# Kernel optimization log

Hardware: AMD Instinct MI355X
Metric: run time of the kernel (lower is better)

The kernel has to match this reference:

```python
import jax, jax.numpy as jnp
import numpy as np

B, C, H, W = 4, 512, 64, 64
IC = C // 2  # inter_plane
EPS = 1e-5


def _conv1x1(x, w, b=None):
    # x: [b,c,h,w], w: [o,c] -> [b,o,h,w]
    y = jnp.einsum('bchw,oc->bohw', x, w)
    if b is not None:
        y = y + b[None, :, None, None]
    return y


def setup_inputs() -> dict:
    key = jax.random.key(0)
    ks = jax.random.split(key, 20)
    rn = lambda i, sh, s=0.02: jax.random.normal(ks[i], sh, jnp.float32) * s
    return {
        'xA': jax.random.normal(ks[0], (B, C, H, W), jnp.float32),
        'wk': rn(1, (IC, C)), 'bk': rn(2, (IC,)),
        'wv': rn(3, (IC, C)), 'bv': rn(4, (IC,)),
        'wq': rn(5, (IC, C)), 'bq': rn(6, (IC,)),
        'wwg': rn(7, (IC, IC)),
        'bn1_g': jnp.ones((IC,), jnp.float32), 'bn1_b': rn(8, (IC,)),
        'bn1_m': rn(9, (IC,)), 'bn1_v': jax.random.uniform(ks[10], (IC,), jnp.float32, 0.5, 1.5),
        'wout': rn(11, (C, IC)), 'bout': rn(12, (C,)),
        'bn2_g': jnp.ones((C,), jnp.float32), 'bn2_b': rn(13, (C,)),
        'bn2_m': rn(14, (C,)), 'bn2_v': jax.random.uniform(ks[15], (C,), jnp.float32, 0.5, 1.5),
    }


def reference(xA, wk, bk, wv, bv, wq, bq, wwg, bn1_g, bn1_b, bn1_m, bn1_v,
              wout, bout, bn2_g, bn2_b, bn2_m, bn2_v):
    b, c, h, w = xA.shape
    n = h * w
    k = _conv1x1(xA, wk, bk).reshape(b, IC, n)   # [b,ic,n]
    v = _conv1x1(xA, wv, bv).reshape(b, IC, n)   # [b,ic,n] (permuted via einsum below)
    q = _conv1x1(xA, wq, bq).reshape(b, IC, n)   # [b,ic,n]
    # AV = softmax(v^T @ q, axis=2): [b,n,n]
    attn = jax.nn.softmax(jnp.einsum('bcn,bcm->bnm', v, q), axis=2)
    av = jnp.einsum('bcn,bnm->bcm', k, attn)     # [b,ic,n]
    # conv1d 1x1 (no bias) + BatchNorm1d (eval mode)
    avw = jnp.einsum('oc,bcn->bon', wwg, av)
    scale1 = bn1_g / jnp.sqrt(bn1_v + EPS)
    avw = (avw - bn1_m[None, :, None]) * scale1[None, :, None] + bn1_b[None, :, None]
    avw = avw.reshape(b, IC, h, w)
    # out conv + BatchNorm2d (eval) + residual + relu
    o = _conv1x1(avw, wout, bout)
    scale2 = bn2_g / jnp.sqrt(bn2_v + EPS)
    o = (o - bn2_m[None, :, None, None]) * scale2[None, :, None, None] + bn2_b[None, :, None, None]
    return jax.nn.relu(o + xA)
```

## Files before the change

kernel.cpp:

```cpp
#include <hip/hip_runtime.h>


#define N_ 4096
#define C_ 512
#define IC_ 256
#define B_ 4

typedef __bf16 bf16_t;
typedef __bf16 bf16x8 __attribute__((ext_vector_type(8)));
typedef __bf16 bf16x4 __attribute__((ext_vector_type(4)));
typedef float f32x4 __attribute__((ext_vector_type(4)));

#define GLD(g, l) __builtin_amdgcn_global_load_lds(                              \
    (const __attribute__((address_space(1))) void*)(g),                          \
    (__attribute__((address_space(3))) void*)(l), 16, 0, 0)

__device__ __forceinline__ void gemm_bt_128x128(
    const bf16_t* __restrict__ A, int lda,
    const bf16_t* __restrict__ Bt, int ldb,
    int K, int m0, int n0,
    bf16_t* smem, f32x4 acc[4][4])
{
    const int tid  = threadIdx.x;
    const int wave = tid >> 6, lane = tid & 63;
    const int wr = (wave >> 1) * 64, wc = (wave & 1) * 64;
    const int q = lane >> 4, l15 = lane & 15;
    const int srow = lane >> 3;
    const int scol = (((lane & 7) ^ (srow & 7)) * 8);
    const int swz  = l15 & 7;

#define GB_STAGE(bi, kt)                                                        \
    do {                                                                        \
        bf16_t* lA = smem + (bi) * 16384;                                       \
        bf16_t* lB = lA + 8192;                                                 \
        _Pragma("unroll")                                                       \
        for (int c = 0; c < 4; ++c) {                                           \
            const int ch = wave * 4 + c;                                        \
            GLD(A  + (size_t)(m0 + ch * 8 + srow) * lda + (kt) + scol,          \
                lA + ch * 512);                                                 \
            GLD(Bt + (size_t)(n0 + ch * 8 + srow) * ldb + (kt) + scol,          \
                lB + ch * 512);                                                 \
        }                                                                       \
    } while (0)

    GB_STAGE(0, 0);
    asm volatile("s_waitcnt vmcnt(0)" ::: "memory");
    __builtin_amdgcn_s_barrier();
    asm volatile("" ::: "memory");

    const int nt = K / 64;
    for (int t = 0; t < nt; ++t) {
        const int cur = t & 1;
        if (t + 1 < nt) GB_STAGE(cur ^ 1, (t + 1) * 64);
        const bf16_t* lsA = smem + cur * 16384;
        const bf16_t* lsB = lsA + 8192;
#pragma unroll
        for (int ks = 0; ks < 2; ++ks) {
            bf16x8 af[4], bfr[4];
            const int co = ((ks * 4 + q) ^ swz) * 8;
#pragma unroll
            for (int i = 0; i < 4; ++i) {
                af[i]  = *(const bf16x8*)&lsA[(wr + i * 16 + l15) * 64 + co];
                bfr[i] = *(const bf16x8*)&lsB[(wc + i * 16 + l15) * 64 + co];
            }
#pragma unroll
            for (int i = 0; i < 4; ++i)
#pragma unroll
                for (int j = 0; j < 4; ++j)
                    acc[i][j] = __builtin_amdgcn_mfma_f32_16x16x32_bf16(
                        af[i], bfr[j], acc[i][j], 0, 0, 0);
        }
        asm volatile("s_waitcnt vmcnt(0)" ::: "memory");
        __builtin_amdgcn_s_barrier();
        asm volatile("" ::: "memory");
    }
#undef GB_STAGE
}

#define ACC_ZERO(acc)                                                           \
    _Pragma("unroll") for (int i = 0; i < 4; ++i)                               \
    _Pragma("unroll") for (int j = 0; j < 4; ++j)                               \
        acc[i][j] = f32x4{0.f, 0.f, 0.f, 0.f};

__global__ __launch_bounds__(256) void prep_k(
    const float* __restrict__ wk, const float* __restrict__ wv,
    const float* __restrict__ wq,
    const float* __restrict__ wwg, const float* __restrict__ wout,
    const float* __restrict__ bout,
    const float* __restrict__ g1, const float* __restrict__ b1,
    const float* __restrict__ m1, const float* __restrict__ v1,
    const float* __restrict__ g2, const float* __restrict__ b2,
    const float* __restrict__ m2, const float* __restrict__ v2,
    bf16_t* __restrict__ Wb3, bf16_t* __restrict__ Wfb,
    float* __restrict__ bfv, float* __restrict__ rowsum)
{
    const int bid = blockIdx.x;
    __shared__ float ws[256];
    __shared__ float red[4];

    if (bid < 1536) {
        const int i = bid * 256 + threadIdx.x;
        float v;
        if      (i < 131072) v = wk[i];
        else if (i < 262144) v = wv[i - 131072];
        else                 v = wq[i - 262144];
        Wb3[i] = (bf16_t)v;
    } else if (bid < 2048) {
        const int o = bid - 1536;
        const int j = threadIdx.x;
        const float s1 = g1[j] * rsqrtf(v1[j] + 1e-5f);
        const float wo = wout[o * 256 + j];
        ws[j] = wo * s1;
        float bp = wo * (b1[j] - m1[j] * s1);
#pragma unroll
        for (int off = 32; off > 0; off >>= 1) bp += __shfl_down(bp, off);
        if ((j & 63) == 0) red[j >> 6] = bp;
        __syncthreads();

        float acc = 0.f;
#pragma unroll 4
        for (int ic = 0; ic < 256; ++ic)
            acc += ws[ic] * wwg[ic * 256 + j];

        const float s2 = g2[o] * rsqrtf(v2[o] + 1e-5f);
        Wfb[o * 256 + j] = (bf16_t)(acc * s2);
        if (j == 0)
            bfv[o] = s2 * (red[0] + red[1] + red[2] + red[3] + bout[o])
                     - s2 * m2[o] + b2[o];
    } else {
        rowsum[(bid - 2048) * 256 + threadIdx.x] = 0.f;
    }
}

__global__ __launch_bounds__(256) void txa_k(
    const float* __restrict__ xA, bf16_t* __restrict__ xAt)
{
    __shared__ float t[32][33];
    const int b = blockIdx.z;
    const int n0 = blockIdx.x * 32, c0 = blockIdx.y * 32;
    const int tx = threadIdx.x, ty = threadIdx.y;
    const float* X = xA + (size_t)b * C_ * N_;
    bf16_t* Y = xAt + (size_t)b * N_ * C_;
#pragma unroll
    for (int r = 0; r < 4; ++r)
        t[ty + r * 8][tx] = X[(size_t)(c0 + ty + r * 8) * N_ + n0 + tx];
    __syncthreads();
#pragma unroll
    for (int r = 0; r < 4; ++r)
        Y[(size_t)(n0 + ty + r * 8) * C_ + c0 + tx] = (bf16_t)t[tx][ty + r * 8];
}

__global__ __launch_bounds__(256) void conv_mfma_k(
    const bf16_t* __restrict__ Wb3,
    const float* __restrict__ bk, const float* __restrict__ bv,
    const float* __restrict__ bq, const bf16_t* __restrict__ xAt,
    bf16_t* __restrict__ Kb, bf16_t* __restrict__ Vt, bf16_t* __restrict__ Qt)
{
    __shared__ bf16_t smem[32768];
    const int which = blockIdx.z % 3, b = blockIdx.z / 3;
    const bf16_t* A = Wb3 + which * 131072;
    const float* bias = (which == 0) ? bk : (which == 1 ? bv : bq);
    const bf16_t* Bt = xAt + (size_t)b * N_ * C_;
    const int n0 = blockIdx.x * 128, m0 = blockIdx.y * 128;

    f32x4 acc[4][4];
    ACC_ZERO(acc);
    gemm_bt_128x128(A, C_, Bt, C_, C_, m0, n0, smem, acc);

    const int lane = threadIdx.x & 63, wave = threadIdx.x >> 6;
    const int q = lane >> 4, l15 = lane & 15;
    const int wr = (wave >> 1) * 64, wc = (wave & 1) * 64;

    if (which == 0) {
        bf16_t* Y = Kb + (size_t)b * IC_ * N_;
#pragma unroll
        for (int i = 0; i < 4; ++i)
#pragma unroll
            for (int r = 0; r < 4; ++r) {
                const int o = m0 + wr + i * 16 + q * 4 + r;
                const float bo = bias[o];
#pragma unroll
                for (int j = 0; j < 4; ++j)
                    Y[(size_t)o * N_ + n0 + wc + j * 16 + l15] =
                        (bf16_t)(acc[i][j][r] + bo);
            }
    } else {
        bf16_t* Y = ((which == 1) ? Vt : Qt) + (size_t)b * N_ * IC_;
#pragma unroll
        for (int i = 0; i < 4; ++i) {
            const int ob = m0 + wr + i * 16 + q * 4;
            float bo[4];
#pragma unroll
            for (int r = 0; r < 4; ++r) bo[r] = bias[ob + r];
#pragma unroll
            for (int j = 0; j < 4; ++j) {
                const int n = n0 + wc + j * 16 + l15;
                bf16x4 v4;
#pragma unroll
                for (int r = 0; r < 4; ++r) v4[r] = (bf16_t)(acc[i][j][r] + bo[r]);
                *(bf16x4*)&Y[(size_t)n * IC_ + ob] = v4;
            }
        }
    }
}

__global__ __launch_bounds__(256) void s_mfma_t_k(
    const bf16_t* __restrict__ Qt, const bf16_t* __restrict__ Vt,
    bf16_t* __restrict__ Pt, float* __restrict__ rowsum)
{
    __shared__ bf16_t smem[32768];
    const int b  = blockIdx.z;
    const int n0 = blockIdx.x * 128;
    const int m0 = blockIdx.y * 128;
    const size_t NIC = (size_t)N_ * IC_;
    const bf16_t* Qb = Qt + (size_t)b * NIC;
    const bf16_t* Vb = Vt + (size_t)b * NIC;
    bf16_t* Pb = Pt + (size_t)b * N_ * N_;
    float* rs = rowsum + b * N_;

    f32x4 acc[4][4];
    ACC_ZERO(acc);
    gemm_bt_128x128(Qb, IC_, Vb, IC_, IC_, m0, n0, smem, acc);

    const int tid = threadIdx.x;
    const int lane = tid & 63, wave = tid >> 6;
    const int q = lane >> 4, l15 = lane & 15;
    const int wr = (wave >> 1) * 64, wc = (wave & 1) * 64;

#pragma unroll
    for (int j = 0; j < 4; ++j) {
        float cs = 0.f;
#pragma unroll
        for (int i = 0; i < 4; ++i)
#pragma unroll
            for (int r = 0; r < 4; ++r) {
                const float e = __expf(acc[i][j][r]);
                cs += e;
                smem[(wr + i * 16 + q * 4 + r) * 136 + wc + j * 16 + l15] = (bf16_t)e;
            }
        cs += __shfl_xor(cs, 16);
        cs += __shfl_xor(cs, 32);
        if (q == 0) atomicAdd(&rs[n0 + wc + j * 16 + l15], cs);
    }
    __syncthreads();

    const int rr = tid >> 4;
    const int cc = (tid & 15) * 8;
#pragma unroll
    for (int p = 0; p < 8; ++p) {
        const int mm = rr + p * 16;
        const bf16x8 v = *(const bf16x8*)&smem[mm * 136 + cc];
        *(bf16x8*)&Pb[(size_t)(m0 + mm) * N_ + n0 + cc] = v;
    }
}

__global__ __launch_bounds__(256) void kscale_k(
    bf16_t* __restrict__ Kb, const float* __restrict__ rowsum)
{
    const size_t i8 = ((size_t)blockIdx.x * 256 + threadIdx.x) * 8;
    const int n = (int)(i8 & (N_ - 1));
    const int b = (int)(i8 >> 20);
    const float* rs = rowsum + b * N_;
    bf16x8 v = *(bf16x8*)&Kb[i8];
    const f32x4 r0 = *(const f32x4*)&rs[n];
    const f32x4 r1 = *(const f32x4*)&rs[n + 4];
#pragma unroll
    for (int k = 0; k < 4; ++k) {
        v[k]     = (bf16_t)((float)v[k]     / r0[k]);
        v[4 + k] = (bf16_t)((float)v[4 + k] / r1[k]);
    }
    *(bf16x8*)&Kb[i8] = v;
}

__global__ __launch_bounds__(256) void av_mfma_k(
    const bf16_t* __restrict__ Pt, const bf16_t* __restrict__ Kb,
    bf16_t* __restrict__ avTb)
{
    __shared__ bf16_t smem[3 * 16384];
    const int b  = blockIdx.z;
    const int m0 = blockIdx.x * 128;
    const int c0 = blockIdx.y * 128;
    const size_t NIC = (size_t)N_ * IC_;
    const bf16_t* Pb  = Pt + (size_t)b * N_ * N_ + (size_t)m0 * N_;
    const bf16_t* Kbb = Kb + (size_t)b * NIC + (size_t)c0 * N_;

    const int tid = threadIdx.x;
    const int wave = tid >> 6, lane = tid & 63;
    const int wr = (wave >> 1) * 64, wc = (wave & 1) * 64;
    const int q = lane >> 4, l15 = lane & 15;
    const int srow = lane >> 3;
    const int scol = (((lane & 7) ^ (srow & 7)) * 8);
    const int swz  = l15 & 7;

    f32x4 acc[4][4];
    ACC_ZERO(acc);

#define AV_STAGE(buf, kt)                                                       \
    do {                                                                        \
        _Pragma("unroll")                                                       \
        for (int c = 0; c < 4; ++c) {                                           \
            const int ch = wave * 4 + c;                                        \
            GLD(Pb  + (size_t)(ch * 8 + srow) * N_ + (kt) + scol,               \
                (buf) + ch * 512);                                              \
            GLD(Kbb + (size_t)(ch * 8 + srow) * N_ + (kt) + scol,               \
                (buf) + 8192 + ch * 512);                                       \
        }                                                                       \
    } while (0)

    const int NT = N_ / 64;
    AV_STAGE(smem, 0);
    AV_STAGE(smem + 16384, 64);

    int bi_c = 0;
    int bi_s = 2;
    for (int t = 0; t < NT; ++t) {
        if (t + 2 < NT) {
            asm volatile("s_waitcnt vmcnt(8)" ::: "memory");
            __builtin_amdgcn_s_barrier();
            asm volatile("" ::: "memory");
            AV_STAGE(smem + bi_s * 16384, (t + 2) * 64);
        } else {
            asm volatile("s_waitcnt vmcnt(0)" ::: "memory");
            __builtin_amdgcn_s_barrier();
            asm volatile("" ::: "memory");
        }
        const bf16_t* lsA = smem + bi_c * 16384;
        const bf16_t* lsB = lsA + 8192;
#pragma unroll
        for (int ks = 0; ks < 2; ++ks) {
            const int co = ((ks * 4 + q) ^ swz) * 8;
            bf16x8 af[4], bfr[4];
#pragma unroll
            for (int i = 0; i < 4; ++i) {
                af[i]  = *(const bf16x8*)&lsA[(wr + i * 16 + l15) * 64 + co];
                bfr[i] = *(const bf16x8*)&lsB[(wc + i * 16 + l15) * 64 + co];
            }
#pragma unroll
            for (int i = 0; i < 4; ++i)
#pragma unroll
                for (int j = 0; j < 4; ++j)
                    acc[i][j] = __builtin_amdgcn_mfma_f32_16x16x32_bf16(
                        af[i], bfr[j], acc[i][j], 0, 0, 0);
        }
        bi_c = (bi_c == 2) ? 0 : bi_c + 1;
        bi_s = (bi_s == 2) ? 0 : bi_s + 1;
    }
#undef AV_STAGE
    __syncthreads();

#pragma unroll
    for (int i = 0; i < 4; ++i)
#pragma unroll
        for (int j = 0; j < 4; ++j)
#pragma unroll
            for (int r = 0; r < 4; ++r)
                smem[(wr + i * 16 + q * 4 + r) * 136 + wc + j * 16 + l15] =
                    (bf16_t)acc[i][j][r];
    __syncthreads();

    bf16_t* Y = avTb + (size_t)b * NIC + (size_t)m0 * IC_ + c0;
    const int rr = tid >> 4;
    const int cc = (tid & 15) * 8;
#pragma unroll
    for (int p = 0; p < 8; ++p) {
        const int mm = rr + p * 16;
        const bf16x8 v = *(const bf16x8*)&smem[mm * 136 + cc];
        *(bf16x8*)&Y[(size_t)mm * IC_ + cc] = v;
    }
}

__global__ __launch_bounds__(256) void out_mfma_k(
    const bf16_t* __restrict__ Wfb, const float* __restrict__ bfv,
    const bf16_t* __restrict__ avTb,
    const float* __restrict__ xA, float* __restrict__ out)
{
    __shared__ bf16_t smem[32768];
    const int b = blockIdx.z;
    const bf16_t* Bt = avTb + (size_t)b * N_ * IC_;
    const int n0 = blockIdx.x * 128, o0 = blockIdx.y * 128;

    f32x4 acc[4][4];
    ACC_ZERO(acc);
    gemm_bt_128x128(Wfb, IC_, Bt, IC_, IC_, o0, n0, smem, acc);

    const int lane = threadIdx.x & 63, wave = threadIdx.x >> 6;
    const int q = lane >> 4, l15 = lane & 15;
    const int wr = (wave >> 1) * 64, wc = (wave & 1) * 64;

#pragma unroll
    for (int i = 0; i < 4; ++i)
#pragma unroll
        for (int r = 0; r < 4; ++r) {
            const int o = o0 + wr + i * 16 + q * 4 + r;
            const float bo = bfv[o];
#pragma unroll
            for (int j = 0; j < 4; ++j) {
                const int n = n0 + wc + j * 16 + l15;
                const size_t idx = ((size_t)b * C_ + o) * N_ + n;
                out[idx] = fmaxf(acc[i][j][r] + bo + xA[idx], 0.f);
            }
        }
}

extern "C" void kernel_launch(void* const* d_in, const int* in_sizes, int n_in,
                              void* d_out, int out_size, void* d_ws, size_t ws_size,
                              hipStream_t stream)
{
    const float* xA    = (const float*)d_in[0];
    const float* wk    = (const float*)d_in[1];
    const float* bk    = (const float*)d_in[2];
    const float* wv    = (const float*)d_in[3];
    const float* bv    = (const float*)d_in[4];
    const float* wq    = (const float*)d_in[5];
    const float* bq    = (const float*)d_in[6];
    const float* wwg   = (const float*)d_in[7];
    const float* bn1_g = (const float*)d_in[8];
    const float* bn1_b = (const float*)d_in[9];
    const float* bn1_m = (const float*)d_in[10];
    const float* bn1_v = (const float*)d_in[11];
    const float* wout  = (const float*)d_in[12];
    const float* bout  = (const float*)d_in[13];
    const float* bn2_g = (const float*)d_in[14];
    const float* bn2_b = (const float*)d_in[15];
    const float* bn2_m = (const float*)d_in[16];
    const float* bn2_v = (const float*)d_in[17];
    float* out = (float*)d_out;

    char* p = (char*)d_ws;
    bf16_t* Wb3    = (bf16_t*)p; p += 786432;
    bf16_t* Wfb    = (bf16_t*)p; p += 262144;
    float*  bfv    = (float*)p;  p += 2048;
    bf16_t* xAt    = (bf16_t*)p;
    bf16_t* avTb   = (bf16_t*)p; p += 16777216;
    bf16_t* Kb     = (bf16_t*)p; p += 8388608;
    bf16_t* Vt     = (bf16_t*)p; p += 8388608;
    bf16_t* Qt     = (bf16_t*)p; p += 8388608;
    float*  rowsum = (float*)p;  p += 65536;
    bf16_t* Pt     = (bf16_t*)p; p += 134217728;

    prep_k<<<2112, 256, 0, stream>>>(wk, wv, wq, wwg, wout, bout,
                                     bn1_g, bn1_b, bn1_m, bn1_v,
                                     bn2_g, bn2_b, bn2_m, bn2_v,
                                     Wb3, Wfb, bfv, rowsum);
    txa_k<<<dim3(N_ / 32, C_ / 32, B_), dim3(32, 8), 0, stream>>>(xA, xAt);
    conv_mfma_k<<<dim3(N_ / 128, IC_ / 128, 3 * B_), 256, 0, stream>>>(
        Wb3, bk, bv, bq, xAt, Kb, Vt, Qt);

    s_mfma_t_k<<<dim3(N_ / 128, N_ / 128, B_), 256, 0, stream>>>(
        Qt, Vt, Pt, rowsum);
    kscale_k<<<2048, 256, 0, stream>>>(Kb, rowsum);
    av_mfma_k<<<dim3(N_ / 128, IC_ / 128, B_), 256, 0, stream>>>(Pt, Kb, avTb);

    out_mfma_k<<<dim3(N_ / 128, C_ / 128, B_), 256, 0, stream>>>(
        Wfb, bfv, avTb, xA, out);
}
```

Measured before the change: 280.5 us.

## Enlarge score GEMM tile to 256x256 with 8 waves and triple-buffered loads

```diff
diff --git a/kernel.cpp b/kernel.cpp
--- a/kernel.cpp
+++ b/kernel.cpp
@@ -204,53 +204,114 @@
     }
 }
 
-__global__ __launch_bounds__(256) void s_mfma_t_k(
+__global__ __launch_bounds__(512, 2) void s_mfma_t_k(
     const bf16_t* __restrict__ Qt, const bf16_t* __restrict__ Vt,
     bf16_t* __restrict__ Pt, float* __restrict__ rowsum)
 {
-    __shared__ bf16_t smem[32768];
+    __shared__ bf16_t smem[49152];
     const int b  = blockIdx.z;
-    const int n0 = blockIdx.x * 128;
-    const int m0 = blockIdx.y * 128;
+    const int n0 = blockIdx.x * 256;
+    const int m0 = blockIdx.y * 256;
     const size_t NIC = (size_t)N_ * IC_;
     const bf16_t* Qb = Qt + (size_t)b * NIC;
     const bf16_t* Vb = Vt + (size_t)b * NIC;
     bf16_t* Pb = Pt + (size_t)b * N_ * N_;
     float* rs = rowsum + b * N_;
 
-    f32x4 acc[4][4];
-    ACC_ZERO(acc);
-    gemm_bt_128x128(Qb, IC_, Vb, IC_, IC_, m0, n0, smem, acc);
-
-    const int tid = threadIdx.x;
-    const int lane = tid & 63, wave = tid >> 6;
+    const int tid  = threadIdx.x;
+    const int wave = tid >> 6, lane = tid & 63;
+    const int wr = wave >> 2;
+    const int wn = wave & 3;
     const int q = lane >> 4, l15 = lane & 15;
-    const int wr = (wave >> 1) * 64, wc = (wave & 1) * 64;
-
-#pragma unroll
-    for (int j = 0; j < 4; ++j) {
-        float cs = 0.f;
-#pragma unroll
-        for (int i = 0; i < 4; ++i)
-#pragma unroll
-            for (int r = 0; r < 4; ++r) {
-                const float e = __expf(acc[i][j][r]);
-                cs += e;
-                smem[(wr + i * 16 + q * 4 + r) * 136 + wc + j * 16 + l15] = (bf16_t)e;
+    const int lr  = lane >> 2;
+    const int swl = ((lane >> 2) & 3) ^ ((lane >> 4) & 3);
+    const int sc8 = ((lane & 3) ^ swl) * 8;
+    const int swr = (l15 & 3) ^ ((l15 >> 2) & 3);
+    const int co  = (q ^ swr) * 8;
+
+    f32x4 acc[8][4];
+#pragma unroll
+    for (int i = 0; i < 8; ++i)
+#pragma unroll
+        for (int j = 0; j < 4; ++j) acc[i][j] = f32x4{0.f, 0.f, 0.f, 0.f};
+
+#define S_STAGE(buf, kt)                                                        \
+    do {                                                                        \
+        _Pragma("unroll")                                                       \
+        for (int c = 0; c < 2; ++c) {                                           \
+            const int ch = wave * 2 + c;                                        \
+            const int gr = ch * 16 + lr;                                        \
+            GLD(Qb + (size_t)(m0 + gr) * IC_ + (kt) + sc8, (buf) + ch * 512);   \
+            GLD(Vb + (size_t)(n0 + gr) * IC_ + (kt) + sc8,                      \
+                (buf) + 8192 + ch * 512);                                       \
+        }                                                                       \
+    } while (0)
+
+    const int NT = IC_ / 32;
+    S_STAGE(smem, 0);
+    S_STAGE(smem + 16384, 32);
+
+    int bc = 0, bs = 2;
+    for (int t = 0; t < NT; ++t) {
+        if (t + 1 < NT) {
+            asm volatile("s_waitcnt vmcnt(4)" ::: "memory");
+        } else {
+            asm volatile("s_waitcnt vmcnt(0)" ::: "memory");
+        }
+        __builtin_amdgcn_s_barrier();
+        asm volatile("" ::: "memory");
+        if (t + 2 < NT) S_STAGE(smem + bs * 16384, (t + 2) * 32);
+
+        const bf16_t* lsA = smem + bc * 16384;
+        const bf16_t* lsB = lsA + 8192;
+        bf16x8 af[8], bf[4];
+#pragma unroll
+        for (int i = 0; i < 8; ++i)
+            af[i] = *(const bf16x8*)&lsA[(wr * 128 + i * 16 + l15) * 32 + co];
+#pragma unroll
+        for (int j = 0; j < 4; ++j)
+            bf[j] = *(const bf16x8*)&lsB[(wn * 64 + j * 16 + l15) * 32 + co];
+#pragma unroll
+        for (int i = 0; i < 8; ++i)
+#pragma unroll
+            for (int j = 0; j < 4; ++j)
+                acc[i][j] = __builtin_amdgcn_mfma_f32_16x16x32_bf16(
+                    af[i], bf[j], acc[i][j], 0, 0, 0);
+        bc = (bc == 2) ? 0 : bc + 1;
+        bs = (bs == 2) ? 0 : bs + 1;
+    }
+#undef S_STAGE
+
+#pragma unroll
+    for (int h = 0; h < 2; ++h) {
+        if ((wn >> 1) == h) {
+#pragma unroll
+            for (int j = 0; j < 4; ++j) {
+                float cs = 0.f;
+#pragma unroll
+                for (int i = 0; i < 8; ++i)
+#pragma unroll
+                    for (int r = 0; r < 4; ++r) {
+                        const float e = __expf(acc[i][j][r]);
+                        cs += e;
+                        smem[(wr * 128 + i * 16 + q * 4 + r) * 136 +
+                             (wn & 1) * 64 + j * 16 + l15] = (bf16_t)e;
+                    }
+                cs += __shfl_xor(cs, 16);
+                cs += __shfl_xor(cs, 32);
+                if (q == 0) atomicAdd(&rs[n0 + wn * 64 + j * 16 + l15], cs);
             }
-        cs += __shfl_xor(cs, 16);
-        cs += __shfl_xor(cs, 32);
-        if (q == 0) atomicAdd(&rs[n0 + wc + j * 16 + l15], cs);
-    }
-    __syncthreads();
-
-    const int rr = tid >> 4;
-    const int cc = (tid & 15) * 8;
-#pragma unroll
-    for (int p = 0; p < 8; ++p) {
-        const int mm = rr + p * 16;
-        const bf16x8 v = *(const bf16x8*)&smem[mm * 136 + cc];
-        *(bf16x8*)&Pb[(size_t)(m0 + mm) * N_ + n0 + cc] = v;
+        }
+        __syncthreads();
+        const int rr0 = tid >> 4;
+        const int cc  = (tid & 15) * 8;
+#pragma unroll
+        for (int pp = 0; pp < 8; ++pp) {
+            const int rr = rr0 + pp * 32;
+            const bf16x8 v = *(const bf16x8*)&smem[rr * 136 + cc];
+            *(bf16x8*)&Pb[(size_t)(m0 + rr) * N_ + n0 + h * 128 + cc] = v;
+        }
+        __syncthreads();
     }
 }
 
@@ -328,12 +389,12 @@
         const bf16_t* lsB = lsA + 8192;
 #pragma unroll
         for (int ks = 0; ks < 2; ++ks) {
-            const int co = ((ks * 4 + q) ^ swz) * 8;
+            const int co2 = ((ks * 4 + q) ^ swz) * 8;
             bf16x8 af[4], bfr[4];
 #pragma unroll
             for (int i = 0; i < 4; ++i) {
-                af[i]  = *(const bf16x8*)&lsA[(wr + i * 16 + l15) * 64 + co];
-                bfr[i] = *(const bf16x8*)&lsB[(wc + i * 16 + l15) * 64 + co];
+                af[i]  = *(const bf16x8*)&lsA[(wr + i * 16 + l15) * 64 + co2];
+                bfr[i] = *(const bf16x8*)&lsB[(wc + i * 16 + l15) * 64 + co2];
             }
 #pragma unroll
             for (int i = 0; i < 4; ++i)
@@ -446,7 +507,7 @@
     conv_mfma_k<<<dim3(N_ / 128, IC_ / 128, 3 * B_), 256, 0, stream>>>(
         Wb3, bk, bv, bq, xAt, Kb, Vt, Qt);
 
-    s_mfma_t_k<<<dim3(N_ / 128, N_ / 128, B_), 256, 0, stream>>>(
+    s_mfma_t_k<<<dim3(N_ / 256, N_ / 256, B_), 512, 0, stream>>>(
         Qt, Vt, Pt, rowsum);
     kscale_k<<<2048, 256, 0, stream>>>(Kb, rowsum);
     av_mfma_k<<<dim3(N_ / 128, IC_ / 128, B_), 256, 0, stream>>>(Pt, Kb, avTb);
```

New measurement: 289.5 us. +3.2%, slower.

## Inline double-buffered async-LDS GEMM in score kernel with smaller shared memory

Applied to the files above, without the earlier changes.

```diff
diff --git a/kernel.cpp b/kernel.cpp
--- a/kernel.cpp
+++ b/kernel.cpp
@@ -208,7 +208,7 @@
     const bf16_t* __restrict__ Qt, const bf16_t* __restrict__ Vt,
     bf16_t* __restrict__ Pt, float* __restrict__ rowsum)
 {
-    __shared__ bf16_t smem[32768];
+    __shared__ bf16_t smem[17408];
     const int b  = blockIdx.z;
     const int n0 = blockIdx.x * 128;
     const int m0 = blockIdx.y * 128;
@@ -218,14 +218,63 @@
     bf16_t* Pb = Pt + (size_t)b * N_ * N_;
     float* rs = rowsum + b * N_;
 
+    const int tid = threadIdx.x;
+    const int wave = tid >> 6, lane = tid & 63;
+    const int q = lane >> 4, l15 = lane & 15;
+    const int wr = (wave >> 1) * 64, wc = (wave & 1) * 64;
+
+    const int rowoff = lane >> 3;
+    const int sA = (lane & 7) ^ rowoff;
+    const int pA = sA >> 2, cA = (sA & 3) * 8;
+    const int rl = l15 >> 1;
+    const int slot_q = ((((l15 & 1) * 4 + q)) ^ rl) * 8;
+
     f32x4 acc[4][4];
     ACC_ZERO(acc);
-    gemm_bt_128x128(Qb, IC_, Vb, IC_, IC_, m0, n0, smem, acc);
-
-    const int tid = threadIdx.x;
-    const int lane = tid & 63, wave = tid >> 6;
-    const int q = lane >> 4, l15 = lane & 15;
-    const int wr = (wave >> 1) * 64, wc = (wave & 1) * 64;
+
+#define S_STAGE(bi, kt)                                                         \
+    do {                                                                        \
+        bf16_t* lA = smem + (bi) * 8192;                                        \
+        bf16_t* lB = lA + 4096;                                                 \
+        _Pragma("unroll")                                                       \
+        for (int e = 0; e < 2; ++e) {                                           \
+            const int R0 = wave * 16 + e * 8;                                   \
+            const int gr = 2 * (R0 + rowoff) + pA;                              \
+            GLD(Qb + (size_t)(m0 + gr) * IC_ + (kt) + cA,                       \
+                lA + R0 * 64 + lane * 8);                                       \
+            GLD(Vb + (size_t)(n0 + gr) * IC_ + (kt) + cA,                       \
+                lB + R0 * 64 + lane * 8);                                       \
+        }                                                                       \
+    } while (0)
+
+    S_STAGE(0, 0);
+    asm volatile("s_waitcnt vmcnt(0)" ::: "memory");
+    __builtin_amdgcn_s_barrier();
+    asm volatile("" ::: "memory");
+
+    const int NT = IC_ / 32;
+    for (int t = 0; t < NT; ++t) {
+        const int cur = t & 1;
+        if (t + 1 < NT) S_STAGE(cur ^ 1, (t + 1) * 32);
+        const bf16_t* lsA = smem + cur * 8192;
+        const bf16_t* lsB = lsA + 4096;
+        bf16x8 af[4], bfr[4];
+#pragma unroll
+        for (int i = 0; i < 4; ++i) {
+            af[i]  = *(const bf16x8*)&lsA[((wr >> 1) + i * 8 + rl) * 64 + slot_q];
+            bfr[i] = *(const bf16x8*)&lsB[((wc >> 1) + i * 8 + rl) * 64 + slot_q];
+        }
+#pragma unroll
+        for (int i = 0; i < 4; ++i)
+#pragma unroll
+            for (int j = 0; j < 4; ++j)
+                acc[i][j] = __builtin_amdgcn_mfma_f32_16x16x32_bf16(
+                    af[i], bfr[j], acc[i][j], 0, 0, 0);
+        asm volatile("s_waitcnt vmcnt(0)" ::: "memory");
+        __builtin_amdgcn_s_barrier();
+        asm volatile("" ::: "memory");
+    }
+#undef S_STAGE
 
 #pragma unroll
     for (int j = 0; j < 4; ++j) {
@@ -328,12 +377,12 @@
         const bf16_t* lsB = lsA + 8192;
 #pragma unroll
         for (int ks = 0; ks < 2; ++ks) {
-            const int co = ((ks * 4 + q) ^ swz) * 8;
+            const int co2 = ((ks * 4 + q) ^ swz) * 8;
             bf16x8 af[4], bfr[4];
 #pragma unroll
             for (int i = 0; i < 4; ++i) {
-                af[i]  = *(const bf16x8*)&lsA[(wr + i * 16 + l15) * 64 + co];
-                bfr[i] = *(const bf16x8*)&lsB[(wc + i * 16 + l15) * 64 + co];
+                af[i]  = *(const bf16x8*)&lsA[(wr + i * 16 + l15) * 64 + co2];
+                bfr[i] = *(const bf16x8*)&lsB[(wc + i * 16 + l15) * 64 + co2];
             }
 #pragma unroll
             for (int i = 0; i < 4; ++i)
```

After: 274.9 us. 1.02x faster.
